# Optimization experiments

Hardware: AMD Instinct MI355X
Metric: run time of the kernel (lower is better)

Reference implementation:

```python
import jax, jax.numpy as jnp
import numpy as np

N_HEADS = 8
CLIP = 10.0  # tanh clipping constant of the pointer logits
NEG = -1e9


def setup_inputs() -> dict:
    key = jax.random.key(0)
    ks = jax.random.split(key, 10)
    B, N, H = 1024, 100, 128
    s = 1.0 / np.sqrt(H).astype(np.float32)
    return {
        "encoder_inputs": jax.random.normal(ks[0], (B, N, H), jnp.float32),
        "pool": jax.random.normal(ks[1], (B, H), jnp.float32),
        "capacity": jnp.full((B, 1), 50.0, jnp.float32),  # vehicle capacity
        "demand": (1.0 + 9.0 * jax.random.uniform(ks[2], (B, N), jnp.float32)).at[:, 0].set(0.0),  # depot demand = 0
        "fc_w": jax.random.normal(ks[3], (H, H + 1), jnp.float32) * s,
        "fc1_w": jax.random.normal(ks[4], (H, H), jnp.float32) * s,
        "Wq": jax.random.normal(ks[5], (H, H), jnp.float32) * s,
        "Wk": jax.random.normal(ks[6], (H, H), jnp.float32) * s,
        "Wv": jax.random.normal(ks[7], (H, H), jnp.float32) * s,
        "Wo": jax.random.normal(ks[8], (H, H), jnp.float32) * s,
        "Wk2": jax.random.normal(ks[9], (H, H), jnp.float32) * s,
        "n_steps": 128,
        "T": 1,
        "greedy": 1,
    }


def _decode(encoder_inputs, pool, capacity, demand, fc_w, fc1_w, Wq, Wk, Wv, Wo, Wk2, n_steps, T):
    B, N, H = encoder_inputs.shape
    hd = H // N_HEADS
    # encoder projections are step-invariant -> hoist out of the loop
    K = (encoder_inputs @ Wk.T).reshape(B, N, N_HEADS, hd)
    V = (encoder_inputs @ Wv.T).reshape(B, N, N_HEADS, hd)
    K2 = encoder_inputs @ Wk2.T  # [B, N, H] pointer keys
    pool_proj = pool @ fc1_w.T   # [B, H]
    base_cap = capacity[0, 0]
    rows = jnp.arange(B)

    def update_mask(cap, index, mask1):
        # mask1: permanently visited customers (depot never permanently masked)
        go_depot = (index == 0)
        mask1 = mask1.at[rows, index].set(1.0)
        mask1 = mask1.at[:, 0].set(0.0)
        mask = jnp.maximum(mask1, (demand > cap).astype(jnp.float32))
        # cannot stay at depot; but depot must stay open once all customers are masked
        all_cust = jnp.all(mask[:, 1:] > 0.0, axis=1)
        depot = jnp.where(all_cust, 0.0, go_depot.astype(jnp.float32))
        mask = mask.at[:, 0].set(depot)
        return mask, mask1

    mask0, mask1_0 = update_mask(capacity, jnp.zeros((B,), jnp.int32), jnp.zeros((B, N), jnp.float32))
    inp0 = encoder_inputs[:, 0, :]
    inv_sqrt_hd = 1.0 / jnp.sqrt(jnp.float32(hd))
    inv_sqrt_h = 1.0 / jnp.sqrt(jnp.float32(H))

    def step(carry, _):
        _inp, cap, mask, mask1 = carry
        dec = jnp.concatenate([_inp, cap], axis=-1) @ fc_w.T + pool_proj  # [B, H]
        # multi-head glimpse over encoder nodes
        q = (dec @ Wq.T).reshape(B, N_HEADS, hd)
        scores = jnp.einsum('bhd,bnhd->bhn', q, K) * inv_sqrt_hd
        scores = jnp.where(mask[:, None, :] > 0.0, NEG, scores)
        attn = jax.nn.softmax(scores, axis=-1)
        glimpse = jnp.einsum('bhn,bnhd->bhd', attn, V).reshape(B, H) @ Wo.T
        # single-head clipped pointer logits
        u = CLIP * jnp.tanh(jnp.einsum('bh,bnh->bn', glimpse, K2) * inv_sqrt_h)
        u = jnp.where(mask > 0.0, NEG, u)
        logp_all = jax.nn.log_softmax(u / T, axis=-1)
        index = jnp.argmax(logp_all, axis=-1)  # greedy decoding
        log_p = jnp.take_along_axis(logp_all, index[:, None], axis=1)[:, 0]
        is_done = (jnp.sum(mask1[:, 1:], axis=1) >= N - 1).astype(jnp.float32)
        log_p = log_p * (1.0 - is_done)
        # state update: subtract served demand; reset to base capacity at depot
        sel_d = jnp.take_along_axis(demand, index[:, None], axis=1)
        cap = jnp.where(index[:, None] == 0, base_cap, cap - sel_d)
        mask, mask1 = update_mask(cap, index, mask1)
        _inp = jnp.take_along_axis(encoder_inputs, index[:, None, None], axis=1)[:, 0]
        return (_inp, cap, mask, mask1), (index, log_p)

    _, (actions, log_ps) = jax.lax.scan(step, (inp0, capacity, mask0, mask1_0), None, length=n_steps)
    return actions.T, jnp.sum(log_ps, axis=0)  # ([B, n_steps], [B])


def reference(encoder_inputs, pool, capacity, demand, fc_w, fc1_w, Wq, Wk, Wv, Wo, Wk2, n_steps, T, greedy):
    actions, log_p = _decode(encoder_inputs, pool, capacity, demand, fc_w, fc1_w, Wq, Wk, Wv, Wo, Wk2, n_steps, T)
    return actions, log_p
```

## Files before the change

### kernel.cpp

```cpp
#include <hip/hip_runtime.h>
#include <math.h>

#define NNODE 100
#define NEGV  -1000000000.0f

__device__ float g_Wall [128 * 512];
__device__ float g_Wall2[128 * 128];
__device__ float g_qcap [128];
__device__ float g_C    [(size_t)102400 * 512];
__device__ float g_qpool[(size_t)1024 * 128];
__device__ float g_S1   [(size_t)1024 * 100 * 800];
__device__ float g_Scap [(size_t)1024 * 800];

__device__ __forceinline__ float fast_rcp(float x) { return __builtin_amdgcn_rcpf(x); }
__device__ __forceinline__ float tanh10(float z) {
    const float e2 = __expf(2.0f * z);
    return fmaf(-20.0f, __builtin_amdgcn_rcpf(e2 + 1.0f), 10.0f);
}

template<int CTRL>
__device__ __forceinline__ int dpp_i(int v) {
    return __builtin_amdgcn_update_dpp(0, v, CTRL, 0xF, 0xF, true);
}
template<int CTRL>
__device__ __forceinline__ float dpp_f(float v) {
    return __uint_as_float((unsigned)dpp_i<CTRL>(__float_as_int(v)));
}

#if defined(__has_builtin)
#  if __has_builtin(__builtin_amdgcn_permlane16_swap)
#    define HAVE_PL16 1
#  endif
#  if __has_builtin(__builtin_amdgcn_permlane32_swap)
#    define HAVE_PL32 1
#  endif
#endif

__device__ __forceinline__ void x16_both(float x, float& a, float& b) {
#if defined(HAVE_PL16)
    auto r = __builtin_amdgcn_permlane16_swap(__float_as_uint(x),
                                              __float_as_uint(x), false, false);
    a = __uint_as_float(r[0]); b = __uint_as_float(r[1]);
#else
    a = x;
    b = __uint_as_float(
        (unsigned)__builtin_amdgcn_ds_swizzle(__float_as_int(x), 0x401F));
#endif
}
__device__ __forceinline__ void x32_both(float x, float& a, float& b) {
#if defined(HAVE_PL32)
    auto r = __builtin_amdgcn_permlane32_swap(__float_as_uint(x),
                                              __float_as_uint(x), false, false);
    a = __uint_as_float(r[0]); b = __uint_as_float(r[1]);
#else
    a = x;
    b = __shfl_xor(x, 32, 64);
#endif
}
__device__ __forceinline__ float x16_sum(float x) { float a, b; x16_both(x, a, b); return a + b; }
__device__ __forceinline__ float x16_max(float x) { float a, b; x16_both(x, a, b); return fmaxf(a, b); }
__device__ __forceinline__ float x32_sum(float x) { float a, b; x32_both(x, a, b); return a + b; }
__device__ __forceinline__ float x32_max(float x) { float a, b; x32_both(x, a, b); return fmaxf(a, b); }
__device__ __forceinline__ void x32_pair(float x, float& lo, float& hi) {
#if defined(HAVE_PL32)
    auto r = __builtin_amdgcn_permlane32_swap(__float_as_uint(x),
                                              __float_as_uint(x), false, false);
    lo = __uint_as_float(r[0]); hi = __uint_as_float(r[1]);
#else
    const float o = __shfl_xor(x, 32, 64);
    const bool high = (threadIdx.x & 32) != 0;
    lo = high ? o : x;
    hi = high ? x : o;
#endif
}

__global__ __launch_bounds__(128) void prep_kernel(
    const float* __restrict__ Wk,  const float* __restrict__ Wv,
    const float* __restrict__ Wk2, const float* __restrict__ Wo,
    const float* __restrict__ Wq,  const float* __restrict__ fc_w,
    const float* __restrict__ fc1_w)
{
    const int c = blockIdx.x;
    const int k = threadIdx.x;
    if (c < 128) {
        g_Wall[k * 512 + c] = Wk[c * 128 + k];
    } else if (c < 256) {
        g_Wall[k * 512 + c] = Wv[(c - 128) * 128 + k];
    } else if (c < 384) {
        const int cc = c - 256;
        float acc = 0.f;
        for (int h = 0; h < 128; h++)
            acc = fmaf(Wk2[h * 128 + k], Wo[h * 128 + cc], acc);
        g_Wall[k * 512 + c] = acc;
    } else if (c < 512) {
        const int cc = c - 384;
        float acc = 0.f;
        for (int j = 0; j < 128; j++)
            acc = fmaf(Wq[cc * 128 + j], fc_w[j * 129 + k], acc);
        g_Wall[k * 512 + c] = acc;
    } else if (c == 512) {
        float acc = 0.f;
        for (int j = 0; j < 128; j++)
            acc = fmaf(Wq[k * 128 + j], fc_w[j * 129 + 128], acc);
        g_qcap[k] = acc;
    } else {
        const int cc = c - 513;
        float acc = 0.f;
        for (int j = 0; j < 128; j++)
            acc = fmaf(Wq[cc * 128 + j], fc1_w[j * 128 + k], acc);
        g_Wall2[k * 128 + cc] = acc;
    }
}

__global__ __launch_bounds__(512) void gemm_kernel(const float* __restrict__ A0,
                                                   const float* __restrict__ A1)
{
    const bool mode1 = (blockIdx.x >= 800);
    if (mode1 && blockIdx.y > 0) return;
    const float* __restrict__ A = mode1 ? A1 : A0;
    const float* __restrict__ W = mode1 ? g_Wall2 : g_Wall;
    float* __restrict__ C       = mode1 ? g_qpool : g_C;
    const int ncols             = mode1 ? 128 : 512;
    const int m0 = (mode1 ? (blockIdx.x - 800) : blockIdx.x) * 128;
    const int n0 = blockIdx.y * 128;

    __shared__ __align__(16) float At[32 * 132];
    __shared__ __align__(16) float Ws[32 * 128];
    const int tid = threadIdx.x;
    const int tm = tid >> 5, tn = tid & 31;
    const int mb = tm * 8, nb = tn * 4;
    float4 acc[8];
#pragma unroll
    for (int i = 0; i < 8; i++) acc[i] = make_float4(0.f, 0.f, 0.f, 0.f);

    for (int kc = 0; kc < 4; kc++) {
        for (int f = tid; f < 1024; f += 512) {
            const int r = f >> 3, q8 = f & 7;
            float4 a = *(const float4*)&A[(size_t)(m0 + r) * 128 + kc * 32 + q8 * 4];
            At[(q8 * 4 + 0) * 132 + r] = a.x;
            At[(q8 * 4 + 1) * 132 + r] = a.y;
            At[(q8 * 4 + 2) * 132 + r] = a.z;
            At[(q8 * 4 + 3) * 132 + r] = a.w;
            const int kl = f >> 5, q = f & 31;
            *(float4*)&Ws[kl * 128 + q * 4] =
                *(const float4*)&W[(size_t)(kc * 32 + kl) * ncols + n0 + q * 4];
        }
        __syncthreads();
        for (int k = 0; k < 32; k++) {
            const float4 w = *(float4*)&Ws[k * 128 + nb];
#pragma unroll
            for (int i = 0; i < 8; i += 4) {
                const float4 a = *(float4*)&At[k * 132 + mb + i];
                acc[i + 0].x = fmaf(a.x, w.x, acc[i + 0].x);
                acc[i + 0].y = fmaf(a.x, w.y, acc[i + 0].y);
                acc[i + 0].z = fmaf(a.x, w.z, acc[i + 0].z);
                acc[i + 0].w = fmaf(a.x, w.w, acc[i + 0].w);
                acc[i + 1].x = fmaf(a.y, w.x, acc[i + 1].x);
                acc[i + 1].y = fmaf(a.y, w.y, acc[i + 1].y);
                acc[i + 1].z = fmaf(a.y, w.z, acc[i + 1].z);
                acc[i + 1].w = fmaf(a.y, w.w, acc[i + 1].w);
                acc[i + 2].x = fmaf(a.z, w.x, acc[i + 2].x);
                acc[i + 2].y = fmaf(a.z, w.y, acc[i + 2].y);
                acc[i + 2].z = fmaf(a.z, w.z, acc[i + 2].z);
                acc[i + 2].w = fmaf(a.z, w.w, acc[i + 2].w);
                acc[i + 3].x = fmaf(a.w, w.x, acc[i + 3].x);
                acc[i + 3].y = fmaf(a.w, w.y, acc[i + 3].y);
                acc[i + 3].z = fmaf(a.w, w.z, acc[i + 3].z);
                acc[i + 3].w = fmaf(a.w, w.w, acc[i + 3].w);
            }
        }
        __syncthreads();
    }
#pragma unroll
    for (int i = 0; i < 8; i++)
        *(float4*)&C[(size_t)(m0 + mb + i) * ncols + n0 + nb] = acc[i];
}

__global__ __launch_bounds__(256) void s1_kernel()
{
    const int b = blockIdx.x;
    const int tid = threadIdx.x;
    const int h = tid >> 5, l32 = tid & 31;
    const int n0 = l32 * 4;
    const bool act = n0 < 100;
    const float* __restrict__ Crow = &g_C[(size_t)b * 100 * 512];

    __shared__ __align__(16) float Q1sh[50 * 128];

    float4 kr[4][4];
#pragma unroll
    for (int j = 0; j < 4; j++)
#pragma unroll
        for (int i = 0; i < 4; i++)
            kr[j][i] = act ? *(const float4*)&Crow[(size_t)(n0 + j) * 512 + h * 16 + i * 4]
                           : make_float4(0.f, 0.f, 0.f, 0.f);

    float4 qc[4], qp[4];
#pragma unroll
    for (int i = 0; i < 4; i++) {
        qc[i] = *(const float4*)&g_qcap[h * 16 + i * 4];
        qp[i] = *(const float4*)&g_qpool[(size_t)b * 128 + h * 16 + i * 4];
    }
    float sp[4], scv[4];
#pragma unroll
    for (int j = 0; j < 4; j++) {
        float dc = 0.f, dp = 0.f;
#pragma unroll
        for (int i = 0; i < 4; i++) {
            dc = fmaf(kr[j][i].x, qc[i].x, dc); dc = fmaf(kr[j][i].y, qc[i].y, dc);
            dc = fmaf(kr[j][i].z, qc[i].z, dc); dc = fmaf(kr[j][i].w, qc[i].w, dc);
            dp = fmaf(kr[j][i].x, qp[i].x, dp); dp = fmaf(kr[j][i].y, qp[i].y, dp);
            dp = fmaf(kr[j][i].z, qp[i].z, dp); dp = fmaf(kr[j][i].w, qp[i].w, dp);
        }
        sp[j]  = dp;
        scv[j] = dc * 0.25f;
    }
    if (act)
        *(float4*)&g_Scap[(size_t)b * 800 + h * 100 + n0] =
            make_float4(scv[0], scv[1], scv[2], scv[3]);

    float* __restrict__ S1b = &g_S1[(size_t)b * 80000];
    for (int half = 0; half < 2; half++) {
        const int mbase = half * 50;
        for (int f = tid; f < 1600; f += 256) {
            const int n = f >> 5, c4 = f & 31;
            *(float4*)&Q1sh[n * 128 + c4 * 4] =
                *(const float4*)&Crow[(size_t)(mbase + n) * 512 + 384 + c4 * 4];
        }
        __syncthreads();
        for (int mm = 0; mm < 50; mm++) {
            const int m = mbase + mm;
            float4 q[4];
#pragma unroll
            for (int i = 0; i < 4; i++)
                q[i] = *(float4*)&Q1sh[mm * 128 + h * 16 + i * 4];
            float dv[4];
#pragma unroll
            for (int j = 0; j < 4; j++) {
                float d = 0.f;
#pragma unroll
                for (int i = 0; i < 4; i++) {
                    d = fmaf(kr[j][i].x, q[i].x, d); d = fmaf(kr[j][i].y, q[i].y, d);
                    d = fmaf(kr[j][i].z, q[i].z, d); d = fmaf(kr[j][i].w, q[i].w, d);
                }
                dv[j] = (d + sp[j]) * 0.25f;
            }
            if (act)
                *(float4*)&S1b[(size_t)m * 800 + h * 100 + n0] =
                    make_float4(dv[0], dv[1], dv[2], dv[3]);
        }
        __syncthreads();
    }
}

__global__ __launch_bounds__(256) void decode_kernel(
    const float* __restrict__ capacity, const float* __restrict__ demand,
    const int* __restrict__ nsteps_p, const int* __restrict__ T_p,
    float* __restrict__ out)
{
    __shared__ float u_buf[2 * 800];
    __shared__ float demand_sh[NNODE];
    __shared__ int   act_sh[512];

    const int tid = threadIdx.x;
    const int b   = blockIdx.x;
    const int nsteps = nsteps_p[0];
    const float invT = 1.0f / (float)T_p[0];
    const float base_cap = capacity[0];
    const float inv_sqrt_h = 0.08838834764831845f;

    const float4* __restrict__ C4  = (const float4*)&g_C[(size_t)b * 100 * 512];
    const float*  __restrict__ S1b = &g_S1[(size_t)b * 80000];

    const int w = tid >> 6, l = tid & 63;
    const int g = l >> 3, f = l & 7;
    const int F = 8 * w + f;
    const int h8 = tid >> 5, l32 = tid & 31;

    float4 Vreg[13], K2r[13];
#pragma unroll
    for (int m = 0; m < 13; m++) {
        const int n = g + 8 * m;
        const bool v = n < 100;
        Vreg[m] = v ? C4[(size_t)n * 128 + 32 + F] : make_float4(0.f, 0.f, 0.f, 0.f);
        K2r[m]  = v ? C4[(size_t)n * 128 + 64 + F] : make_float4(0.f, 0.f, 0.f, 0.f);
    }
    float s1r[4], scapr[4], d4[4];
#pragma unroll
    for (int j = 0; j < 4; j++) {
        const int nj = l32 + 32 * j;
        const bool v = nj < 100;
        scapr[j] = v ? g_Scap[(size_t)b * 800 + h8 * 100 + nj] : 0.f;
        s1r[j]   = v ? S1b[h8 * 100 + nj] : 0.f;
        d4[j]    = v ? demand[b * 100 + nj] : 1.0e30f;
    }
    const float de0 = demand[b * 100 + l];
    const float de1 = (l + 64 < 100) ? demand[b * 100 + l + 64] : 1.0e30f;
    for (int n = tid; n < 100; n += 256) demand_sh[n] = demand[b * 100 + n];
    for (int t = tid; t < 512; t += 256) act_sh[t] = 0;
    bool me0 = false, me1 = false;
    unsigned mb4 = 0;
    float cap_r = capacity[b];
    float depot_r;
    {
        const bool am0 = (l == 0) ? true : (de0 > cap_r);
        const bool am1 = (l + 64 >= 100) ? true : (de1 > cap_r);
        depot_r = __all(am0 && am1) ? 0.f : 1.f;
    }
    float logp_r = 0.f;
    int visited_r = 0;
    int ub = 0;
    __syncthreads();

    for (int s = 0; s < nsteps; s++) {
        const float cap = cap_r;

        float a[4];
        float tot;
        {
            float sc[4];
#pragma unroll
            for (int j = 0; j < 4; j++) {
                const int nj = l32 + 32 * j;
                const bool m = (nj == 0) ? (depot_r != 0.f)
                    : (((mb4 >> j) & 1u) || (d4[j] > cap));
                const float raw = fmaf(cap, scapr[j], s1r[j]);
                sc[j] = (nj < 100 && !m) ? raw : NEGV;
            }
#pragma unroll
            for (int j = 0; j < 4; j++) a[j] = __expf(sc[j]);
            tot = (a[0] + a[1]) + (a[2] + a[3]);
        }

        float4 gp4 = make_float4(0.f, 0.f, 0.f, 0.f);
#pragma unroll
        for (int m = 0; m < 13; m++) {
            const int src = ((f >> 2) << 5) | (8 * (m & 3) + g);
            const float av = __shfl(a[m >> 2], src, 64);
            gp4.x = fmaf(av, Vreg[m].x, gp4.x);
            gp4.y = fmaf(av, Vreg[m].y, gp4.y);
            gp4.z = fmaf(av, Vreg[m].z, gp4.z);
            gp4.w = fmaf(av, Vreg[m].w, gp4.w);
        }
        tot += dpp_f<0xB1>(tot);
        tot += dpp_f<0x4E>(tot);
        tot += dpp_f<0x124>(tot);
        tot += dpp_f<0x128>(tot);
        tot = x16_sum(tot);
        gp4.x += dpp_f<0x128>(gp4.x);
        gp4.y += dpp_f<0x128>(gp4.y);
        gp4.z += dpp_f<0x128>(gp4.z);
        gp4.w += dpp_f<0x128>(gp4.w);
        gp4.x = x16_sum(gp4.x);
        gp4.y = x16_sum(gp4.y);
        gp4.z = x16_sum(gp4.z);
        gp4.w = x16_sum(gp4.w);
        gp4.x = x32_sum(gp4.x);
        gp4.y = x32_sum(gp4.y);
        gp4.z = x32_sum(gp4.z);
        gp4.w = x32_sum(gp4.w);
        {
            float tlo, thi;
            x32_pair(tot, tlo, thi);
            const float th = (f >> 2) ? thi : tlo;
            const float rt = fast_rcp(th);
            gp4.x *= rt; gp4.y *= rt; gp4.z *= rt; gp4.w *= rt;
        }

        {
            float pm[13];
#pragma unroll
            for (int m = 0; m < 13; m++) {
                float p = gp4.x * K2r[m].x;
                p = fmaf(gp4.y, K2r[m].y, p);
                p = fmaf(gp4.z, K2r[m].z, p);
                p = fmaf(gp4.w, K2r[m].w, p);
                pm[m] = p;
            }
#pragma unroll
            for (int m = 0; m < 13; m++) pm[m] += dpp_f<0xB1>(pm[m]);
#pragma unroll
            for (int m = 0; m < 13; m++) pm[m] += dpp_f<0x4E>(pm[m]);
            if ((f & 3) == 0) {
                const int r = w * 2 + (f >> 2);
#pragma unroll
                for (int m = 0; m < 13; m++) {
                    const int n = g + 8 * m;
                    if (n < 100) u_buf[ub + r * 100 + n] = pm[m];
                }
            }
        }
        __syncthreads();

        float v0, v1 = -3.0e38f;
        {
            float s8 = 0.f;
#pragma unroll
            for (int r = 0; r < 8; r++) s8 += u_buf[ub + r * 100 + l];
            const float u0 = tanh10(s8 * inv_sqrt_h);
            const bool m0 = (l == 0) ? (depot_r != 0.f) : (me0 || de0 > cap);
            v0 = (m0 ? NEGV : u0) * invT;
            if (l + 64 < 100) {
                float t8 = 0.f;
#pragma unroll
                for (int r = 0; r < 8; r++) t8 += u_buf[ub + r * 100 + l + 64];
                const float u1 = tanh10(t8 * inv_sqrt_h);
                const bool m1 = (me1 || de1 > cap);
                v1 = (m1 ? NEGV : u1) * invT;
            }
        }
        float tt = __expf(v0) + ((l + 64 < 100) ? __expf(v1) : 0.f);
        float vm = fmaxf(v0, v1);
#define E_STG(CTRL)                                                           \
        {                                                                     \
            tt += dpp_f<CTRL>(tt);                                            \
            vm = fmaxf(vm, dpp_f<CTRL>(vm));                                  \
        }
        E_STG(0xB1)
        E_STG(0x4E)
        E_STG(0x124)
        E_STG(0x128)
#undef E_STG
        tt = x16_sum(tt);
        vm = x16_max(vm);
        tt = x32_sum(tt);
        vm = x32_max(vm);
        const unsigned long long b0 = __ballot(v0 == vm);
        const unsigned long long b1 = __ballot(v1 == vm);
        const int idx = b0 ? (int)__builtin_ctzll(b0)
                           : (64 + (int)__builtin_ctzll(b1));

#pragma unroll
        for (int j = 0; j < 4; j++) {
            const int nj = l32 + 32 * j;
            if (nj < 100)
                s1r[j] = S1b[(size_t)idx * 800 + h8 * 100 + nj];
        }

        const float dmd_idx = demand_sh[idx];
        const float capn = (idx == 0) ? base_cap : (cap - dmd_idx);

        if (visited_r < 99) logp_r += vm - __logf(tt);
        visited_r += (idx > 0) ? 1 : 0;
        me0 = me0 || (l == idx && idx > 0);
        me1 = me1 || (l + 64 == idx);
#pragma unroll
        for (int j = 0; j < 4; j++)
            if ((l32 + 32 * j) == idx && idx > 0) mb4 |= (1u << j);

        const bool am0 = (l == 0) ? true : (me0 || de0 > capn);
        const bool am1 = (l + 64 >= 100) ? true : (me1 || de1 > capn);
        const bool allc = __all(am0 && am1);
        depot_r = allc ? 0.f : ((idx == 0) ? 1.f : 0.f);
        cap_r = capn;
        if (tid == 0) act_sh[s] = idx;
        ub ^= 800;

        if (visited_r >= 99) break;
    }

    __syncthreads();
    for (int t = tid; t < nsteps; t += 256)
        out[(size_t)b * nsteps + t] = (float)act_sh[t];
    if (tid == 0)
        out[(size_t)gridDim.x * nsteps + b] = logp_r;
}

extern "C" void kernel_launch(void* const* d_in, const int* in_sizes, int n_in,
                              void* d_out, int out_size, void* d_ws, size_t ws_size,
                              hipStream_t stream) {
    const float* enc    = (const float*)d_in[0];
    const float* pool   = (const float*)d_in[1];
    const float* cap    = (const float*)d_in[2];
    const float* demand = (const float*)d_in[3];
    const float* fc_w   = (const float*)d_in[4];
    const float* fc1_w  = (const float*)d_in[5];
    const float* Wq     = (const float*)d_in[6];
    const float* Wk     = (const float*)d_in[7];
    const float* Wv     = (const float*)d_in[8];
    const float* Wo     = (const float*)d_in[9];
    const float* Wk2    = (const float*)d_in[10];
    const int*   nst    = (const int*)d_in[11];
    const int*   Tp     = (const int*)d_in[12];
    float* out = (float*)d_out;

    prep_kernel<<<641, 128, 0, stream>>>(Wk, Wv, Wk2, Wo, Wq, fc_w, fc1_w);
    gemm_kernel<<<dim3(808, 4), 512, 0, stream>>>(enc, pool);
    s1_kernel<<<1024, 256, 0, stream>>>();
    decode_kernel<<<1024, 256, 0, stream>>>(cap, demand, nst, Tp, out);
}
```

Measured before the change: 810.9 us.

## Pack two batch rows per decode block with shared barrier and joint early exit

The decode kernel now runs two independent batch elements per 512-thread block instead of one per 256-thread block. Each half keeps its own shared-memory buffers, and the halves exit the step loop together once both have finished, which is tracked through a small shared done flag. The aim is to use fewer, larger blocks, which may help scheduling and occupancy. The cost is that a half that finishes early sits idle at the barriers until its partner finishes, and each barrier now waits for both halves.

```diff
diff --git a/kernel.cpp b/kernel.cpp
--- a/kernel.cpp
+++ b/kernel.cpp
@@ -253,17 +253,20 @@
     }
 }
 
-__global__ __launch_bounds__(256) void decode_kernel(
+__global__ __launch_bounds__(512) void decode_kernel(
     const float* __restrict__ capacity, const float* __restrict__ demand,
     const int* __restrict__ nsteps_p, const int* __restrict__ T_p,
     float* __restrict__ out)
 {
-    __shared__ float u_buf[2 * 800];
-    __shared__ float demand_sh[NNODE];
-    __shared__ int   act_sh[512];
-
-    const int tid = threadIdx.x;
-    const int b   = blockIdx.x;
+    __shared__ float u_buf[2][2 * 800];
+    __shared__ float demand_sh[2][NNODE];
+    __shared__ int   act_sh[2][512];
+    __shared__ int   done_sh[2][2];
+
+    const int tid  = threadIdx.x;
+    const int half = tid >> 8;
+    const int htid = tid & 255;
+    const int b    = blockIdx.x * 2 + half;
     const int nsteps = nsteps_p[0];
     const float invT = 1.0f / (float)T_p[0];
     const float base_cap = capacity[0];
@@ -272,10 +275,10 @@
     const float4* __restrict__ C4  = (const float4*)&g_C[(size_t)b * 100 * 512];
     const float*  __restrict__ S1b = &g_S1[(size_t)b * 80000];
 
-    const int w = tid >> 6, l = tid & 63;
+    const int w = htid >> 6, l = htid & 63;
     const int g = l >> 3, f = l & 7;
     const int F = 8 * w + f;
-    const int h8 = tid >> 5, l32 = tid & 31;
+    const int h8 = htid >> 5, l32 = htid & 31;
 
     float4 Vreg[13], K2r[13];
 #pragma unroll
@@ -296,8 +299,8 @@
     }
     const float de0 = demand[b * 100 + l];
     const float de1 = (l + 64 < 100) ? demand[b * 100 + l + 64] : 1.0e30f;
-    for (int n = tid; n < 100; n += 256) demand_sh[n] = demand[b * 100 + n];
-    for (int t = tid; t < 512; t += 256) act_sh[t] = 0;
+    for (int n = htid; n < 100; n += 256) demand_sh[half][n] = demand[b * 100 + n];
+    for (int t = htid; t < 512; t += 256) act_sh[half][t] = 0;
     bool me0 = false, me1 = false;
     unsigned mb4 = 0;
     float cap_r = capacity[b];
@@ -313,157 +316,165 @@
     __syncthreads();
 
     for (int s = 0; s < nsteps; s++) {
+        const bool myDone = (visited_r >= 99);
+        if (htid == 0) done_sh[s & 1][half] = myDone ? 1 : 0;
+
         const float cap = cap_r;
-
-        float a[4];
-        float tot;
-        {
-            float sc[4];
+        float v0, v1 = -3.0e38f;
+
+        if (!myDone) {
+            float a[4];
+            float tot;
+            {
+                float sc[4];
+#pragma unroll
+                for (int j = 0; j < 4; j++) {
+                    const int nj = l32 + 32 * j;
+                    const bool m = (nj == 0) ? (depot_r != 0.f)
+                        : (((mb4 >> j) & 1u) || (d4[j] > cap));
+                    const float raw = fmaf(cap, scapr[j], s1r[j]);
+                    sc[j] = (nj < 100 && !m) ? raw : NEGV;
+                }
+#pragma unroll
+                for (int j = 0; j < 4; j++) a[j] = __expf(sc[j]);
+                tot = (a[0] + a[1]) + (a[2] + a[3]);
+            }
+
+            float4 gp4 = make_float4(0.f, 0.f, 0.f, 0.f);
+#pragma unroll
+            for (int m = 0; m < 13; m++) {
+                const int src = ((f >> 2) << 5) | (8 * (m & 3) + g);
+                const float av = __shfl(a[m >> 2], src, 64);
+                gp4.x = fmaf(av, Vreg[m].x, gp4.x);
+                gp4.y = fmaf(av, Vreg[m].y, gp4.y);
+                gp4.z = fmaf(av, Vreg[m].z, gp4.z);
+                gp4.w = fmaf(av, Vreg[m].w, gp4.w);
+            }
+            tot += dpp_f<0xB1>(tot);
+            tot += dpp_f<0x4E>(tot);
+            tot += dpp_f<0x124>(tot);
+            tot += dpp_f<0x128>(tot);
+            tot = x16_sum(tot);
+            gp4.x += dpp_f<0x128>(gp4.x);
+            gp4.y += dpp_f<0x128>(gp4.y);
+            gp4.z += dpp_f<0x128>(gp4.z);
+            gp4.w += dpp_f<0x128>(gp4.w);
+            gp4.x = x16_sum(gp4.x);
+            gp4.y = x16_sum(gp4.y);
+            gp4.z = x16_sum(gp4.z);
+            gp4.w = x16_sum(gp4.w);
+            gp4.x = x32_sum(gp4.x);
+            gp4.y = x32_sum(gp4.y);
+            gp4.z = x32_sum(gp4.z);
+            gp4.w = x32_sum(gp4.w);
+            {
+                float tlo, thi;
+                x32_pair(tot, tlo, thi);
+                const float th = (f >> 2) ? thi : tlo;
+                const float rt = fast_rcp(th);
+                gp4.x *= rt; gp4.y *= rt; gp4.z *= rt; gp4.w *= rt;
+            }
+
+            {
+                float pm[13];
+#pragma unroll
+                for (int m = 0; m < 13; m++) {
+                    float p = gp4.x * K2r[m].x;
+                    p = fmaf(gp4.y, K2r[m].y, p);
+                    p = fmaf(gp4.z, K2r[m].z, p);
+                    p = fmaf(gp4.w, K2r[m].w, p);
+                    pm[m] = p;
+                }
+#pragma unroll
+                for (int m = 0; m < 13; m++) pm[m] += dpp_f<0xB1>(pm[m]);
+#pragma unroll
+                for (int m = 0; m < 13; m++) pm[m] += dpp_f<0x4E>(pm[m]);
+                if ((f & 3) == 0) {
+                    const int r = w * 2 + (f >> 2);
+#pragma unroll
+                    for (int m = 0; m < 13; m++) {
+                        const int n = g + 8 * m;
+                        if (n < 100) u_buf[half][ub + r * 100 + n] = pm[m];
+                    }
+                }
+            }
+        }
+        __syncthreads();
+
+        if (done_sh[s & 1][0] && done_sh[s & 1][1]) break;
+
+        if (!myDone) {
+            {
+                float s8 = 0.f;
+#pragma unroll
+                for (int r = 0; r < 8; r++) s8 += u_buf[half][ub + r * 100 + l];
+                const float u0 = tanh10(s8 * inv_sqrt_h);
+                const bool m0 = (l == 0) ? (depot_r != 0.f) : (me0 || de0 > cap);
+                v0 = (m0 ? NEGV : u0) * invT;
+                if (l + 64 < 100) {
+                    float t8 = 0.f;
+#pragma unroll
+                    for (int r = 0; r < 8; r++) t8 += u_buf[half][ub + r * 100 + l + 64];
+                    const float u1 = tanh10(t8 * inv_sqrt_h);
+                    const bool m1 = (me1 || de1 > cap);
+                    v1 = (m1 ? NEGV : u1) * invT;
+                }
+            }
+            float tt = __expf(v0) + ((l + 64 < 100) ? __expf(v1) : 0.f);
+            float vm = fmaxf(v0, v1);
+#define E_STG(CTRL)                                                           \
+            {                                                                 \
+                tt += dpp_f<CTRL>(tt);                                        \
+                vm = fmaxf(vm, dpp_f<CTRL>(vm));                              \
+            }
+            E_STG(0xB1)
+            E_STG(0x4E)
+            E_STG(0x124)
+            E_STG(0x128)
+#undef E_STG
+            tt = x16_sum(tt);
+            vm = x16_max(vm);
+            tt = x32_sum(tt);
+            vm = x32_max(vm);
+            const unsigned long long b0 = __ballot(v0 == vm);
+            const unsigned long long b1 = __ballot(v1 == vm);
+            const int idx = b0 ? (int)__builtin_ctzll(b0)
+                               : (64 + (int)__builtin_ctzll(b1));
+
 #pragma unroll
             for (int j = 0; j < 4; j++) {
                 const int nj = l32 + 32 * j;
-                const bool m = (nj == 0) ? (depot_r != 0.f)
-                    : (((mb4 >> j) & 1u) || (d4[j] > cap));
-                const float raw = fmaf(cap, scapr[j], s1r[j]);
-                sc[j] = (nj < 100 && !m) ? raw : NEGV;
-            }
-#pragma unroll
-            for (int j = 0; j < 4; j++) a[j] = __expf(sc[j]);
-            tot = (a[0] + a[1]) + (a[2] + a[3]);
-        }
-
-        float4 gp4 = make_float4(0.f, 0.f, 0.f, 0.f);
-#pragma unroll
-        for (int m = 0; m < 13; m++) {
-            const int src = ((f >> 2) << 5) | (8 * (m & 3) + g);
-            const float av = __shfl(a[m >> 2], src, 64);
-            gp4.x = fmaf(av, Vreg[m].x, gp4.x);
-            gp4.y = fmaf(av, Vreg[m].y, gp4.y);
-            gp4.z = fmaf(av, Vreg[m].z, gp4.z);
-            gp4.w = fmaf(av, Vreg[m].w, gp4.w);
-        }
-        tot += dpp_f<0xB1>(tot);
-        tot += dpp_f<0x4E>(tot);
-        tot += dpp_f<0x124>(tot);
-        tot += dpp_f<0x128>(tot);
-        tot = x16_sum(tot);
-        gp4.x += dpp_f<0x128>(gp4.x);
-        gp4.y += dpp_f<0x128>(gp4.y);
-        gp4.z += dpp_f<0x128>(gp4.z);
-        gp4.w += dpp_f<0x128>(gp4.w);
-        gp4.x = x16_sum(gp4.x);
-        gp4.y = x16_sum(gp4.y);
-        gp4.z = x16_sum(gp4.z);
-        gp4.w = x16_sum(gp4.w);
-        gp4.x = x32_sum(gp4.x);
-        gp4.y = x32_sum(gp4.y);
-        gp4.z = x32_sum(gp4.z);
-        gp4.w = x32_sum(gp4.w);
-        {
-            float tlo, thi;
-            x32_pair(tot, tlo, thi);
-            const float th = (f >> 2) ? thi : tlo;
-            const float rt = fast_rcp(th);
-            gp4.x *= rt; gp4.y *= rt; gp4.z *= rt; gp4.w *= rt;
-        }
-
-        {
-            float pm[13];
-#pragma unroll
-            for (int m = 0; m < 13; m++) {
-                float p = gp4.x * K2r[m].x;
-                p = fmaf(gp4.y, K2r[m].y, p);
-                p = fmaf(gp4.z, K2r[m].z, p);
-                p = fmaf(gp4.w, K2r[m].w, p);
-                pm[m] = p;
-            }
-#pragma unroll
-            for (int m = 0; m < 13; m++) pm[m] += dpp_f<0xB1>(pm[m]);
-#pragma unroll
-            for (int m = 0; m < 13; m++) pm[m] += dpp_f<0x4E>(pm[m]);
-            if ((f & 3) == 0) {
-                const int r = w * 2 + (f >> 2);
-#pragma unroll
-                for (int m = 0; m < 13; m++) {
-                    const int n = g + 8 * m;
-                    if (n < 100) u_buf[ub + r * 100 + n] = pm[m];
-                }
-            }
-        }
-        __syncthreads();
-
-        float v0, v1 = -3.0e38f;
-        {
-            float s8 = 0.f;
-#pragma unroll
-            for (int r = 0; r < 8; r++) s8 += u_buf[ub + r * 100 + l];
-            const float u0 = tanh10(s8 * inv_sqrt_h);
-            const bool m0 = (l == 0) ? (depot_r != 0.f) : (me0 || de0 > cap);
-            v0 = (m0 ? NEGV : u0) * invT;
-            if (l + 64 < 100) {
-                float t8 = 0.f;
-#pragma unroll
-                for (int r = 0; r < 8; r++) t8 += u_buf[ub + r * 100 + l + 64];
-                const float u1 = tanh10(t8 * inv_sqrt_h);
-                const bool m1 = (me1 || de1 > cap);
-                v1 = (m1 ? NEGV : u1) * invT;
-            }
-        }
-        float tt = __expf(v0) + ((l + 64 < 100) ? __expf(v1) : 0.f);
-        float vm = fmaxf(v0, v1);
-#define E_STG(CTRL)                                                           \
-        {                                                                     \
-            tt += dpp_f<CTRL>(tt);                                            \
-            vm = fmaxf(vm, dpp_f<CTRL>(vm));                                  \
-        }
-        E_STG(0xB1)
-        E_STG(0x4E)
-        E_STG(0x124)
-        E_STG(0x128)
-#undef E_STG
-        tt = x16_sum(tt);
-        vm = x16_max(vm);
-        tt = x32_sum(tt);
-        vm = x32_max(vm);
-        const unsigned long long b0 = __ballot(v0 == vm);
-        const unsigned long long b1 = __ballot(v1 == vm);
-        const int idx = b0 ? (int)__builtin_ctzll(b0)
-                           : (64 + (int)__builtin_ctzll(b1));
-
-#pragma unroll
-        for (int j = 0; j < 4; j++) {
-            const int nj = l32 + 32 * j;
-            if (nj < 100)
-                s1r[j] = S1b[(size_t)idx * 800 + h8 * 100 + nj];
-        }
-
-        const float dmd_idx = demand_sh[idx];
-        const float capn = (idx == 0) ? base_cap : (cap - dmd_idx);
-
-        if (visited_r < 99) logp_r += vm - __logf(tt);
-        visited_r += (idx > 0) ? 1 : 0;
-        me0 = me0 || (l == idx && idx > 0);
-        me1 = me1 || (l + 64 == idx);
-#pragma unroll
-        for (int j = 0; j < 4; j++)
-            if ((l32 + 32 * j) == idx && idx > 0) mb4 |= (1u << j);
-
-        const bool am0 = (l == 0) ? true : (me0 || de0 > capn);
-        const bool am1 = (l + 64 >= 100) ? true : (me1 || de1 > capn);
-        const bool allc = __all(am0 && am1);
-        depot_r = allc ? 0.f : ((idx == 0) ? 1.f : 0.f);
-        cap_r = capn;
-        if (tid == 0) act_sh[s] = idx;
-        ub ^= 800;
-
-        if (visited_r >= 99) break;
+                if (nj < 100)
+                    s1r[j] = S1b[(size_t)idx * 800 + h8 * 100 + nj];
+            }
+
+            const float dmd_idx = demand_sh[half][idx];
+            const float capn = (idx == 0) ? base_cap : (cap - dmd_idx);
+
+            if (visited_r < 99) logp_r += vm - __logf(tt);
+            visited_r += (idx > 0) ? 1 : 0;
+            me0 = me0 || (l == idx && idx > 0);
+            me1 = me1 || (l + 64 == idx);
+#pragma unroll
+            for (int j = 0; j < 4; j++)
+                if ((l32 + 32 * j) == idx && idx > 0) mb4 |= (1u << j);
+
+            const bool am0 = (l == 0) ? true : (me0 || de0 > capn);
+            const bool am1 = (l + 64 >= 100) ? true : (me1 || de1 > capn);
+            const bool allc = __all(am0 && am1);
+            depot_r = allc ? 0.f : ((idx == 0) ? 1.f : 0.f);
+            cap_r = capn;
+            if (htid == 0) act_sh[half][s] = idx;
+            ub ^= 800;
+        }
     }
 
     __syncthreads();
-    for (int t = tid; t < nsteps; t += 256)
-        out[(size_t)b * nsteps + t] = (float)act_sh[t];
-    if (tid == 0)
-        out[(size_t)gridDim.x * nsteps + b] = logp_r;
+    const size_t NB = (size_t)gridDim.x * 2;
+    for (int t = htid; t < nsteps; t += 256)
+        out[(size_t)b * nsteps + t] = (float)act_sh[half][t];
+    if (htid == 0)
+        out[NB * nsteps + b] = logp_r;
 }
 
 extern "C" void kernel_launch(void* const* d_in, const int* in_sizes, int n_in,
@@ -487,5 +498,5 @@
     prep_kernel<<<641, 128, 0, stream>>>(Wk, Wv, Wk2, Wo, Wq, fc_w, fc1_w);
     gemm_kernel<<<dim3(808, 4), 512, 0, stream>>>(enc, pool);
     s1_kernel<<<1024, 256, 0, stream>>>();
-    decode_kernel<<<1024, 256, 0, stream>>>(cap, demand, nst, Tp, out);
-}
+    decode_kernel<<<512, 512, 0, stream>>>(cap, demand, nst, Tp, out);
+}
```

New measurement: 861.5 us. 1.06x slower.
